# Kernel optimization log

Measured on AMD Instinct MI355X. Metric: run time of the kernel, lower is better.

Reference implementation:

```python
import jax, jax.numpy as jnp
import numpy as np

L1 = 3072
L2 = 15
L3 = 32
COUNT = 8
KAN_G = 3   # grid intervals
KAN_K = 3   # spline order


def _bspline_basis(x, grid, k):
    """Cox-de Boor B-spline basis. x: [B, in], grid: [in, G+2k+1] -> [B, in, G+k]."""
    x = x[:, :, None]                      # [B, in, 1]
    g = grid[None]                         # [1, in, M]
    B0 = ((x >= g[:, :, :-1]) & (x < g[:, :, 1:])).astype(x.dtype)
    for d in range(1, k + 1):
        B0 = ((x - g[:, :, : -(d + 1)]) / (g[:, :, d:-1] - g[:, :, : -(d + 1)]) * B0[:, :, :-1]
              + (g[:, :, d + 1:] - x) / (g[:, :, d + 1:] - g[:, :, 1:-d]) * B0[:, :, 1:])
    return B0  # [B, in, G+k]


def setup_inputs() -> dict:
    key = jax.random.key(0)
    ks = jax.random.split(key, 9)
    B = 16384
    in_dim = L2 * 2            # 30
    out_dim = L3 * COUNT       # 256
    x = jax.random.normal(ks[0], (B, L1), jnp.float32) * 0.1
    ls_indices = jax.random.randint(ks[1], (B,), 0, COUNT, dtype=jnp.int32)
    l1_w = jax.random.normal(ks[2], ((L2 + 1) * COUNT, L1), jnp.float32) / np.sqrt(L1).astype(np.float32)
    l1_b = jax.random.normal(ks[3], ((L2 + 1) * COUNT,), jnp.float32) * 0.01
    l1f_w = jax.random.normal(ks[4], (L2 + 1, L1), jnp.float32) / np.sqrt(L1).astype(np.float32)
    l1f_b = jnp.zeros((L2 + 1,), jnp.float32)
    # KAN layer: uniform extended grid on [-1,1], G+2k+1 = 10 knots per input dim
    h = 2.0 / KAN_G
    g1 = jnp.arange(-KAN_K, KAN_G + KAN_K + 1, dtype=jnp.float32) * h - 1.0
    kan_grid = jnp.tile(g1[None], (in_dim, 1))                      # [30, 10]
    kan_coef = jax.random.normal(ks[5], (in_dim, out_dim, KAN_G + KAN_K), jnp.float32) * 0.1
    kan_scale_base = jax.random.normal(ks[6], (in_dim, out_dim), jnp.float32) / np.sqrt(in_dim).astype(np.float32)
    kan_scale_sp = jnp.ones((in_dim, out_dim), jnp.float32)
    out_w = jax.random.normal(ks[7], (COUNT, L3), jnp.float32) / np.sqrt(L3).astype(np.float32)
    out_b = jnp.zeros((COUNT,), jnp.float32)
    return dict(x=x, ls_indices=ls_indices, l1_w=l1_w, l1_b=l1_b, l1f_w=l1f_w, l1f_b=l1f_b,
                kan_grid=kan_grid, kan_coef=kan_coef, kan_scale_base=kan_scale_base,
                kan_scale_sp=kan_scale_sp, out_w=out_w, out_b=out_b)


def reference(x, ls_indices, l1_w, l1_b, l1f_w, l1f_b, kan_grid, kan_coef,
              kan_scale_base, kan_scale_sp, out_w, out_b):
    B = x.shape[0]
    idx = ls_indices.reshape(-1) + jnp.arange(B, dtype=ls_indices.dtype) * COUNT  # [B]
    # l1: dense over all stacks, then gather the selected stack row per sample
    l1s = (x @ l1_w.T + l1_b).reshape(B * COUNT, L2 + 1)
    l1c = l1s[idx]                                  # [B, L2+1]
    l1f = x @ l1f_w.T + l1f_b                       # [B, L2+1]
    l1c_, l1c_out = l1c[:, :L2], l1c[:, L2:]
    l1f_, l1f_out = l1f[:, :L2], l1f[:, L2:]
    l1x = l1c_ + l1f_                               # [B, L2]
    l1x = jnp.clip(jnp.concatenate([l1x * l1x * (127.0 / 128.0), l1x], axis=1), 0.0, 1.0)  # [B, 2*L2]
    # KAN layer (single KANLayer, 30 -> 256): silu base + B-spline, summed over inputs
    basis = _bspline_basis(l1x, kan_grid, KAN_K)    # [B, 30, G+k]
    w_sp = kan_coef * kan_scale_sp[:, :, None]      # fold scale into coef -> [30, 256, G+k]
    l2s = (jnp.einsum('bi,io->bo', jax.nn.silu(l1x), kan_scale_base)
           + jnp.einsum('bik,iok->bo', basis, w_sp))  # [B, 256]
    l2c = l2s.reshape(B * COUNT, L3)[idx]           # [B, L3]
    l2x = jnp.clip(l2c, 0.0, 1.0)
    l3s = (l2x @ out_w.T + out_b).reshape(B * COUNT, 1)
    l3c = l3s[idx]                                  # [B, 1]
    return l3c + l1f_out + l1c_out
```

## Files before the change

kernel.cpp:

```cpp
#include <hip/hip_runtime.h>
#include <hip/hip_bf16.h>
#include <math.h>

#define NB 16384
#define KD 3072
#define TPB 256

typedef __attribute__((ext_vector_type(8))) short bf16x8;
typedef __attribute__((ext_vector_type(4))) float f32x4;

#define WS_W_OFF 66816
#define WS_WK_OFF 951552

__device__ __forceinline__ unsigned short f2bf(float f) {
    unsigned u = __float_as_uint(f);
    u += 0x7FFFu + ((u >> 16) & 1u);
    return (unsigned short)(u >> 16);
}

__global__ void k0a(const float* __restrict__ l1_w, const float* __restrict__ l1f_w,
                    unsigned short* __restrict__ W) {
    int g = blockIdx.x * TPB + threadIdx.x;
    int e = g * 4;
    const float* src = (e < 128 * KD) ? (l1_w + e) : (l1f_w + (e - 128 * KD));
    float4 v = *(const float4*)src;
    int2 o;
    o.x = (unsigned)f2bf(v.x) | ((unsigned)f2bf(v.y) << 16);
    o.y = (unsigned)f2bf(v.z) | ((unsigned)f2bf(v.w) << 16);
    *(int2*)(W + e) = o;
}

__global__ void k0b(const float* __restrict__ coef, const float* __restrict__ sb,
                    const float* __restrict__ sp, unsigned short* __restrict__ Wk,
                    int* __restrict__ meta) {
    int o = blockIdx.x;
    int k = threadIdx.x;
    if (o == 0 && k < 16) meta[k] = 0;
    if (k >= 224) return;
    float val = 0.f;
    if (k < 30) {
        val = sb[k * 256 + o];
    } else if (k >= 32 && k < 212) {
        int t = k - 32;
        int i = t / 6;
        int kk = t - i * 6;
        val = coef[((size_t)i * 256 + o) * 6 + kk] * sp[i * 256 + o];
    }
    Wk[o * 224 + k] = f2bf(val);
}

__global__ void k1a(const int* __restrict__ ls, int* __restrict__ meta) {
    int r = blockIdx.x * TPB + threadIdx.x;
    int bb = ls[r];
    int lane = threadIdx.x & 63;
    for (int q = 0; q < 8; q++) {
        unsigned long long mask = __ballot(bb == q);
        if (mask != 0ull) {
            int leader = __ffsll((unsigned long long)mask) - 1;
            if (lane == leader) atomicAdd(&meta[q], (int)__popcll(mask));
        }
    }
}

__global__ void k1b(int* __restrict__ meta) {
    if (threadIdx.x == 0 && blockIdx.x == 0) {
        int po = 0;
        for (int q = 0; q < 8; q++) {
            meta[16 + q] = po;
            po += (meta[q] + 31) & ~31;
        }
        meta[24] = po;
    }
}

__global__ void k1c(const int* __restrict__ ls, int* __restrict__ meta) {
    int r = blockIdx.x * TPB + threadIdx.x;
    int bb = ls[r];
    int lane = threadIdx.x & 63;
    int* cursor = meta + 8;
    const int* po = meta + 16;
    int* idxL = meta + 32;
    for (int q = 0; q < 8; q++) {
        unsigned long long mask = __ballot(bb == q);
        if (mask != 0ull) {
            int leader = __ffsll((unsigned long long)mask) - 1;
            int base = 0;
            if (lane == leader) base = atomicAdd(&cursor[q], (int)__popcll(mask));
            base = __shfl(base, leader);
            if (bb == q) {
                int rank = (int)__popcll(mask & ((1ull << lane) - 1ull));
                idxL[po[q] + base + rank] = r;
            }
        }
    }
}

__global__ __launch_bounds__(TPB, 2) void k2_main(
    const float* __restrict__ x, const int* __restrict__ meta,
    const unsigned short* __restrict__ W, const unsigned short* __restrict__ WkG,
    const float* __restrict__ l1_b, const float* __restrict__ l1f_b,
    const float* __restrict__ out_w, const float* __restrict__ out_b,
    float* __restrict__ out)
{
    __shared__ int s_po[9];
    __shared__ int s_rows[32];
    __shared__ int s_valid[32];
    __shared__ unsigned short Ab[32][64];
    __shared__ unsigned short Bb[32][64];
    __shared__ float hS[32][33];
    __shared__ unsigned short uL[32][232];
    __shared__ unsigned short WkS[32][232];
    __shared__ float sPart[2][32];

    int tid = threadIdx.x;
    if (tid < 9) s_po[tid] = meta[16 + tid];
    __syncthreads();
    int slot0 = blockIdx.x * 32;
    if (slot0 >= s_po[8]) return;
    int b = 0;
    while (b < 7 && slot0 >= s_po[b + 1]) b++;
    int bcnt = meta[b];
    if (tid < 32) {
        int slot = slot0 + tid;
        int rel = slot - s_po[b];
        int valid = (rel < bcnt) ? 1 : 0;
        const int* idxL = meta + 32;
        s_rows[tid] = idxL[valid ? slot : s_po[b]];
        s_valid[tid] = valid;
    }
    __syncthreads();

    int w = tid >> 6, lane = tid & 63;
    int mt = w & 1, nt = w >> 1;
    int quad = lane >> 4, l16 = lane & 15;
    int sm = tid >> 3, seg = tid & 7;

    const float4* xp = (const float4*)(x + (size_t)s_rows[sm] * KD) + seg * 2;
    int wrow = (sm < 16) ? (b * 16 + sm) : (112 + sm);
    const int4* wp = (const int4*)(W + (size_t)wrow * KD) + seg;

    unsigned short* aWr = &Ab[sm][(seg ^ (sm & 7)) * 8];
    unsigned short* bWr = &Bb[sm][(seg ^ (sm & 7)) * 8];
    int arow = mt * 16 + l16;
    int brow = nt * 16 + l16;

    f32x4 acc = {0.f, 0.f, 0.f, 0.f};
    for (int kt = 0; kt < 48; kt++) {
        float4 a0 = xp[kt * 16];
        float4 a1 = xp[kt * 16 + 1];
        int4 bv = wp[kt * 8];
        int4 av;
        av.x = (unsigned)f2bf(a0.x) | ((unsigned)f2bf(a0.y) << 16);
        av.y = (unsigned)f2bf(a0.z) | ((unsigned)f2bf(a0.w) << 16);
        av.z = (unsigned)f2bf(a1.x) | ((unsigned)f2bf(a1.y) << 16);
        av.w = (unsigned)f2bf(a1.z) | ((unsigned)f2bf(a1.w) << 16);
        __syncthreads();
        *(int4*)aWr = av;
        *(int4*)bWr = bv;
        __syncthreads();
#pragma unroll
        for (int ks = 0; ks < 2; ks++) {
            int blkA = ((ks * 4 + quad) ^ (arow & 7)) * 8;
            int blkB = ((ks * 4 + quad) ^ (brow & 7)) * 8;
            bf16x8 af = *(const bf16x8*)(&Ab[arow][blkA]);
            bf16x8 bfv = *(const bf16x8*)(&Bb[brow][blkB]);
            acc = __builtin_amdgcn_mfma_f32_16x16x32_bf16(af, bfv, acc, 0, 0, 0);
        }
    }

    {
        int col = nt * 16 + l16;
        float bias = (col < 16) ? l1_b[b * 16 + col] : l1f_b[col - 16];
        int rbase = mt * 16 + quad * 4;
        hS[rbase + 0][col] = acc[0] + bias;
        hS[rbase + 1][col] = acc[1] + bias;
        hS[rbase + 2][col] = acc[2] + bias;
        hS[rbase + 3][col] = acc[3] + bias;
    }
    __syncthreads();

    if (tid < 32) {
        unsigned* z = (unsigned*)&uL[tid][212];
        z[0] = 0; z[1] = 0; z[2] = 0; z[3] = 0; z[4] = 0; z[5] = 0;
        *(unsigned*)&uL[tid][30] = 0;
    }
    for (int item = tid; item < 480; item += TPB) {
        int row = item / 15;
        int ii = item - row * 15;
        float v = hS[row][ii] + hS[row][16 + ii];
        float xs = fminf(v * v * (127.f / 128.f), 1.f);
        float xl = fminf(fmaxf(v, 0.f), 1.f);
#pragma unroll
        for (int which = 0; which < 2; which++) {
            float xv = which ? xl : xs;
            int i = which ? (15 + ii) : ii;
            float sg = 1.f / (1.f + __expf(-xv));
            uL[row][i] = f2bf(xv * sg);
            float s = xv * 1.5f + 4.5f;
            int j = (int)s;
            float f = s - (float)j;
            float omf = 1.f - f;
            float f2 = f * f, f3 = f2 * f;
            float N0 = omf * omf * omf * (1.f / 6.f);
            float N1 = (3.f * f3 - 6.f * f2 + 4.f) * (1.f / 6.f);
            float N2 = (-3.f * f3 + 3.f * f2 + 3.f * f + 1.f) * (1.f / 6.f);
            float N3 = f3 * (1.f / 6.f);
            float b1 = (j == 4) ? N0 : 0.f;
            float b2 = (j == 4) ? N1 : ((j == 5) ? N0 : 0.f);
            float b3 = (j == 4) ? N2 : ((j == 5) ? N1 : N0);
            float b4 = (j == 4) ? N3 : ((j == 5) ? N2 : N1);
            float b5 = (j == 5) ? N3 : ((j == 6) ? N2 : 0.f);
            unsigned* dst = (unsigned*)&uL[row][32 + i * 6];
            dst[0] = ((unsigned)f2bf(b1) << 16);
            dst[1] = (unsigned)f2bf(b2) | ((unsigned)f2bf(b3) << 16);
            dst[2] = (unsigned)f2bf(b4) | ((unsigned)f2bf(b5) << 16);
        }
    }
    for (int c = tid; c < 448; c += TPB) {
        int row = c / 14;
        int cc = c - row * 14;
        const int4* src = (const int4*)(WkG + ((size_t)(b * 32 + row)) * 224 + cc * 16);
        int4 v0 = src[0];
        int4 v1 = src[1];
        int4* dst = (int4*)&WkS[row][cc * 16];
        dst[0] = v0;
        dst[1] = v1;
    }
    __syncthreads();

    f32x4 acc2 = {0.f, 0.f, 0.f, 0.f};
    const unsigned short* uRd = &uL[mt * 16 + l16][quad * 8];
    const unsigned short* wRd = &WkS[nt * 16 + l16][quad * 8];
#pragma unroll
    for (int ks = 0; ks < 7; ks++) {
        bf16x8 uf = *(const bf16x8*)(uRd + ks * 32);
        bf16x8 wf = *(const bf16x8*)(wRd + ks * 32);
        acc2 = __builtin_amdgcn_mfma_f32_16x16x32_bf16(uf, wf, acc2, 0, 0, 0);
    }

    float ow = out_w[b * 32 + nt * 16 + l16];
    float p0 = fminf(fmaxf(acc2[0], 0.f), 1.f) * ow;
    float p1 = fminf(fmaxf(acc2[1], 0.f), 1.f) * ow;
    float p2 = fminf(fmaxf(acc2[2], 0.f), 1.f) * ow;
    float p3 = fminf(fmaxf(acc2[3], 0.f), 1.f) * ow;
#pragma unroll
    for (int off = 1; off < 16; off <<= 1) {
        p0 += __shfl_xor(p0, off);
        p1 += __shfl_xor(p1, off);
        p2 += __shfl_xor(p2, off);
        p3 += __shfl_xor(p3, off);
    }
    if (l16 == 0) {
        int rbase = mt * 16 + quad * 4;
        sPart[nt][rbase + 0] = p0;
        sPart[nt][rbase + 1] = p1;
        sPart[nt][rbase + 2] = p2;
        sPart[nt][rbase + 3] = p3;
    }
    __syncthreads();
    if (tid < 32 && s_valid[tid]) {
        float res = sPart[0][tid] + sPart[1][tid] + out_b[b] + hS[tid][15] + hS[tid][31];
        out[s_rows[tid]] = res;
    }
}

extern "C" void kernel_launch(void* const* d_in, const int* in_sizes, int n_in,
                              void* d_out, int out_size, void* d_ws, size_t ws_size,
                              hipStream_t stream) {
    (void)in_sizes; (void)n_in; (void)out_size; (void)ws_size;
    const float* x     = (const float*)d_in[0];
    const int*   ls    = (const int*)d_in[1];
    const float* l1_w  = (const float*)d_in[2];
    const float* l1_b  = (const float*)d_in[3];
    const float* l1f_w = (const float*)d_in[4];
    const float* l1f_b = (const float*)d_in[5];
    const float* coef  = (const float*)d_in[7];
    const float* sb    = (const float*)d_in[8];
    const float* sp    = (const float*)d_in[9];
    const float* ow    = (const float*)d_in[10];
    const float* ob    = (const float*)d_in[11];
    float* out = (float*)d_out;

    char* ws = (char*)d_ws;
    int* meta = (int*)ws;
    unsigned short* W  = (unsigned short*)(ws + WS_W_OFF);
    unsigned short* Wk = (unsigned short*)(ws + WS_WK_OFF);

    hipLaunchKernelGGL(k0a, dim3(432), dim3(TPB), 0, stream, l1_w, l1f_w, W);
    hipLaunchKernelGGL(k0b, dim3(256), dim3(TPB), 0, stream, coef, sb, sp, Wk, meta);
    hipLaunchKernelGGL(k1a, dim3(64), dim3(TPB), 0, stream, ls, meta);
    hipLaunchKernelGGL(k1b, dim3(1), dim3(64), 0, stream, meta);
    hipLaunchKernelGGL(k1c, dim3(64), dim3(TPB), 0, stream, ls, meta);
    hipLaunchKernelGGL(k2_main, dim3(520), dim3(TPB), 0, stream,
                       x, meta, W, Wk, l1_b, l1f_b, ow, ob, out);
}
```

Baseline: 366.2 us.

## Fuse preprocessing kernels and double-buffer the main GEMM loop with register prefetch

Merges the weight-conversion, KAN-weight packing and histogram kernels into one launch, with per-block partial counts replacing global atomics and reduced in k1b. The main GEMM loop now double-buffers its LDS tiles and prefetches the next k-tiles into registers, dropping one barrier per step. LDS is aliased between the GEMM buffers and the KAN stage, and launch bounds are raised to 3 blocks per SM to lift occupancy. This trades more register pressure for better latency hiding.

```diff
diff --git a/kernel.cpp b/kernel.cpp
--- a/kernel.cpp
+++ b/kernel.cpp
@@ -9,8 +9,9 @@
 typedef __attribute__((ext_vector_type(8))) short bf16x8;
 typedef __attribute__((ext_vector_type(4))) float f32x4;
 
-#define WS_W_OFF 66816
-#define WS_WK_OFF 951552
+#define WS_PART_OFF 66688
+#define WS_W_OFF 69632
+#define WS_WK_OFF 954368
 
 __device__ __forceinline__ unsigned short f2bf(float f) {
     unsigned u = __float_as_uint(f);
@@ -18,56 +19,73 @@
     return (unsigned short)(u >> 16);
 }
 
-__global__ void k0a(const float* __restrict__ l1_w, const float* __restrict__ l1f_w,
-                    unsigned short* __restrict__ W) {
-    int g = blockIdx.x * TPB + threadIdx.x;
-    int e = g * 4;
-    const float* src = (e < 128 * KD) ? (l1_w + e) : (l1f_w + (e - 128 * KD));
-    float4 v = *(const float4*)src;
-    int2 o;
-    o.x = (unsigned)f2bf(v.x) | ((unsigned)f2bf(v.y) << 16);
-    o.y = (unsigned)f2bf(v.z) | ((unsigned)f2bf(v.w) << 16);
-    *(int2*)(W + e) = o;
-}
-
-__global__ void k0b(const float* __restrict__ coef, const float* __restrict__ sb,
-                    const float* __restrict__ sp, unsigned short* __restrict__ Wk,
-                    int* __restrict__ meta) {
-    int o = blockIdx.x;
-    int k = threadIdx.x;
-    if (o == 0 && k < 16) meta[k] = 0;
-    if (k >= 224) return;
-    float val = 0.f;
-    if (k < 30) {
-        val = sb[k * 256 + o];
-    } else if (k >= 32 && k < 212) {
-        int t = k - 32;
-        int i = t / 6;
-        int kk = t - i * 6;
-        val = coef[((size_t)i * 256 + o) * 6 + kk] * sp[i * 256 + o];
-    }
-    Wk[o * 224 + k] = f2bf(val);
-}
-
-__global__ void k1a(const int* __restrict__ ls, int* __restrict__ meta) {
-    int r = blockIdx.x * TPB + threadIdx.x;
-    int bb = ls[r];
-    int lane = threadIdx.x & 63;
-    for (int q = 0; q < 8; q++) {
-        unsigned long long mask = __ballot(bb == q);
-        if (mask != 0ull) {
-            int leader = __ffsll((unsigned long long)mask) - 1;
-            if (lane == leader) atomicAdd(&meta[q], (int)__popcll(mask));
-        }
-    }
-}
-
-__global__ void k1b(int* __restrict__ meta) {
-    if (threadIdx.x == 0 && blockIdx.x == 0) {
+__global__ void k_pre(const float* __restrict__ l1_w, const float* __restrict__ l1f_w,
+                      unsigned short* __restrict__ W,
+                      const float* __restrict__ coef, const float* __restrict__ sb,
+                      const float* __restrict__ sp, unsigned short* __restrict__ Wk,
+                      const int* __restrict__ ls, int* __restrict__ part) {
+    __shared__ int cnt[8];
+    int bid = blockIdx.x;
+    int tid = threadIdx.x;
+    if (bid < 432) {
+        int g = bid * TPB + tid;
+        int e = g * 4;
+        const float* src = (e < 128 * KD) ? (l1_w + e) : (l1f_w + (e - 128 * KD));
+        float4 v = *(const float4*)src;
+        int2 o;
+        o.x = (unsigned)f2bf(v.x) | ((unsigned)f2bf(v.y) << 16);
+        o.y = (unsigned)f2bf(v.z) | ((unsigned)f2bf(v.w) << 16);
+        *(int2*)(W + e) = o;
+    } else if (bid < 688) {
+        int o = bid - 432;
+        int k = tid;
+        if (k < 224) {
+            float val = 0.f;
+            if (k < 30) {
+                val = sb[k * 256 + o];
+            } else if (k >= 32 && k < 212) {
+                int t = k - 32;
+                int i = t / 6;
+                int kk = t - i * 6;
+                val = coef[((size_t)i * 256 + o) * 6 + kk] * sp[i * 256 + o];
+            }
+            Wk[o * 224 + k] = f2bf(val);
+        }
+    } else {
+        int j = bid - 688;
+        int r = j * TPB + tid;
+        int bb = ls[r];
+        if (tid < 8) cnt[tid] = 0;
+        __syncthreads();
+        int lane = tid & 63;
+        for (int q = 0; q < 8; q++) {
+            unsigned long long mask = __ballot(bb == q);
+            if (mask != 0ull) {
+                int leader = __ffsll((unsigned long long)mask) - 1;
+                if (lane == leader) atomicAdd(&cnt[q], (int)__popcll(mask));
+            }
+        }
+        __syncthreads();
+        if (tid < 8) part[j * 8 + tid] = cnt[tid];
+    }
+}
+
+__global__ void k1b(const int* __restrict__ part, int* __restrict__ meta) {
+    __shared__ int sc[8];
+    int tid = threadIdx.x;
+    if (tid < 8) {
+        int s = 0;
+        for (int j = 0; j < 64; j++) s += part[j * 8 + tid];
+        sc[tid] = s;
+        meta[tid] = s;
+        meta[8 + tid] = 0;
+    }
+    __syncthreads();
+    if (tid == 0) {
         int po = 0;
         for (int q = 0; q < 8; q++) {
             meta[16 + q] = po;
-            po += (meta[q] + 31) & ~31;
+            po += (sc[q] + 31) & ~31;
         }
         meta[24] = po;
     }
@@ -95,7 +113,7 @@
     }
 }
 
-__global__ __launch_bounds__(TPB, 2) void k2_main(
+__global__ __launch_bounds__(TPB, 3) void k2_main(
     const float* __restrict__ x, const int* __restrict__ meta,
     const unsigned short* __restrict__ W, const unsigned short* __restrict__ WkG,
     const float* __restrict__ l1_b, const float* __restrict__ l1f_b,
@@ -105,12 +123,14 @@
     __shared__ int s_po[9];
     __shared__ int s_rows[32];
     __shared__ int s_valid[32];
-    __shared__ unsigned short Ab[32][64];
-    __shared__ unsigned short Bb[32][64];
     __shared__ float hS[32][33];
-    __shared__ unsigned short uL[32][232];
-    __shared__ unsigned short WkS[32][232];
     __shared__ float sPart[2][32];
+    __shared__ char smem[29696];
+
+    unsigned short* Abuf = (unsigned short*)smem;
+    unsigned short* Bbuf = (unsigned short*)(smem + 8192);
+    unsigned short* uL   = (unsigned short*)smem;
+    unsigned short* WkS  = (unsigned short*)(smem + 14848);
 
     int tid = threadIdx.x;
     if (tid < 9) s_po[tid] = meta[16 + tid];
@@ -139,32 +159,64 @@
     int wrow = (sm < 16) ? (b * 16 + sm) : (112 + sm);
     const int4* wp = (const int4*)(W + (size_t)wrow * KD) + seg;
 
-    unsigned short* aWr = &Ab[sm][(seg ^ (sm & 7)) * 8];
-    unsigned short* bWr = &Bb[sm][(seg ^ (sm & 7)) * 8];
+    int wrOff = sm * 64 + ((seg ^ (sm & 7)) * 8);
     int arow = mt * 16 + l16;
     int brow = nt * 16 + l16;
+    int rdA = arow * 64;
+    int rdB = brow * 64;
+
+    float4 a00 = xp[0],  a01 = xp[1];  int4 b0 = wp[0];
+    float4 a10 = xp[16], a11 = xp[17]; int4 b1 = wp[8];
 
     f32x4 acc = {0.f, 0.f, 0.f, 0.f};
-    for (int kt = 0; kt < 48; kt++) {
-        float4 a0 = xp[kt * 16];
-        float4 a1 = xp[kt * 16 + 1];
-        int4 bv = wp[kt * 8];
-        int4 av;
-        av.x = (unsigned)f2bf(a0.x) | ((unsigned)f2bf(a0.y) << 16);
-        av.y = (unsigned)f2bf(a0.z) | ((unsigned)f2bf(a0.w) << 16);
-        av.z = (unsigned)f2bf(a1.x) | ((unsigned)f2bf(a1.y) << 16);
-        av.w = (unsigned)f2bf(a1.z) | ((unsigned)f2bf(a1.w) << 16);
-        __syncthreads();
-        *(int4*)aWr = av;
-        *(int4*)bWr = bv;
-        __syncthreads();
-#pragma unroll
-        for (int ks = 0; ks < 2; ks++) {
-            int blkA = ((ks * 4 + quad) ^ (arow & 7)) * 8;
-            int blkB = ((ks * 4 + quad) ^ (brow & 7)) * 8;
-            bf16x8 af = *(const bf16x8*)(&Ab[arow][blkA]);
-            bf16x8 bfv = *(const bf16x8*)(&Bb[brow][blkB]);
-            acc = __builtin_amdgcn_mfma_f32_16x16x32_bf16(af, bfv, acc, 0, 0, 0);
+    for (int kt = 0; kt < 48; kt += 2) {
+        {
+            int4 av;
+            av.x = (unsigned)f2bf(a00.x) | ((unsigned)f2bf(a00.y) << 16);
+            av.y = (unsigned)f2bf(a00.z) | ((unsigned)f2bf(a00.w) << 16);
+            av.z = (unsigned)f2bf(a01.x) | ((unsigned)f2bf(a01.y) << 16);
+            av.w = (unsigned)f2bf(a01.z) | ((unsigned)f2bf(a01.w) << 16);
+            int4 bv = b0;
+            if (kt < 46) {
+                a00 = xp[(kt + 2) * 16];
+                a01 = xp[(kt + 2) * 16 + 1];
+                b0  = wp[(kt + 2) * 8];
+            }
+            *(int4*)(Abuf + wrOff) = av;
+            *(int4*)(Bbuf + wrOff) = bv;
+            __syncthreads();
+#pragma unroll
+            for (int ks = 0; ks < 2; ks++) {
+                int blkA = ((ks * 4 + quad) ^ (arow & 7)) * 8;
+                int blkB = ((ks * 4 + quad) ^ (brow & 7)) * 8;
+                bf16x8 af  = *(const bf16x8*)(Abuf + rdA + blkA);
+                bf16x8 bfv = *(const bf16x8*)(Bbuf + rdB + blkB);
+                acc = __builtin_amdgcn_mfma_f32_16x16x32_bf16(af, bfv, acc, 0, 0, 0);
+            }
+        }
+        {
+            int4 av;
+            av.x = (unsigned)f2bf(a10.x) | ((unsigned)f2bf(a10.y) << 16);
+            av.y = (unsigned)f2bf(a10.z) | ((unsigned)f2bf(a10.w) << 16);
+            av.z = (unsigned)f2bf(a11.x) | ((unsigned)f2bf(a11.y) << 16);
+            av.w = (unsigned)f2bf(a11.z) | ((unsigned)f2bf(a11.w) << 16);
+            int4 bv = b1;
+            if (kt < 45) {
+                a10 = xp[(kt + 3) * 16];
+                a11 = xp[(kt + 3) * 16 + 1];
+                b1  = wp[(kt + 3) * 8];
+            }
+            *(int4*)(Abuf + 2048 + wrOff) = av;
+            *(int4*)(Bbuf + 2048 + wrOff) = bv;
+            __syncthreads();
+#pragma unroll
+            for (int ks = 0; ks < 2; ks++) {
+                int blkA = ((ks * 4 + quad) ^ (arow & 7)) * 8;
+                int blkB = ((ks * 4 + quad) ^ (brow & 7)) * 8;
+                bf16x8 af  = *(const bf16x8*)(Abuf + 2048 + rdA + blkA);
+                bf16x8 bfv = *(const bf16x8*)(Bbuf + 2048 + rdB + blkB);
+                acc = __builtin_amdgcn_mfma_f32_16x16x32_bf16(af, bfv, acc, 0, 0, 0);
+            }
         }
     }
 
@@ -180,9 +232,9 @@
     __syncthreads();
 
     if (tid < 32) {
-        unsigned* z = (unsigned*)&uL[tid][212];
+        unsigned* z = (unsigned*)(uL + tid * 232 + 212);
         z[0] = 0; z[1] = 0; z[2] = 0; z[3] = 0; z[4] = 0; z[5] = 0;
-        *(unsigned*)&uL[tid][30] = 0;
+        *(unsigned*)(uL + tid * 232 + 30) = 0;
     }
     for (int item = tid; item < 480; item += TPB) {
         int row = item / 15;
@@ -195,7 +247,7 @@
             float xv = which ? xl : xs;
             int i = which ? (15 + ii) : ii;
             float sg = 1.f / (1.f + __expf(-xv));
-            uL[row][i] = f2bf(xv * sg);
+            uL[row * 232 + i] = f2bf(xv * sg);
             float s = xv * 1.5f + 4.5f;
             int j = (int)s;
             float f = s - (float)j;
@@ -210,7 +262,7 @@
             float b3 = (j == 4) ? N2 : ((j == 5) ? N1 : N0);
             float b4 = (j == 4) ? N3 : ((j == 5) ? N2 : N1);
             float b5 = (j == 5) ? N3 : ((j == 6) ? N2 : 0.f);
-            unsigned* dst = (unsigned*)&uL[row][32 + i * 6];
+            unsigned* dst = (unsigned*)(uL + row * 232 + 32 + i * 6);
             dst[0] = ((unsigned)f2bf(b1) << 16);
             dst[1] = (unsigned)f2bf(b2) | ((unsigned)f2bf(b3) << 16);
             dst[2] = (unsigned)f2bf(b4) | ((unsigned)f2bf(b5) << 16);
@@ -222,15 +274,15 @@
         const int4* src = (const int4*)(WkG + ((size_t)(b * 32 + row)) * 224 + cc * 16);
         int4 v0 = src[0];
         int4 v1 = src[1];
-        int4* dst = (int4*)&WkS[row][cc * 16];
+        int4* dst = (int4*)(WkS + row * 232 + cc * 16);
         dst[0] = v0;
         dst[1] = v1;
     }
     __syncthreads();
 
     f32x4 acc2 = {0.f, 0.f, 0.f, 0.f};
-    const unsigned short* uRd = &uL[mt * 16 + l16][quad * 8];
-    const unsigned short* wRd = &WkS[nt * 16 + l16][quad * 8];
+    const unsigned short* uRd = uL + (mt * 16 + l16) * 232 + quad * 8;
+    const unsigned short* wRd = WkS + (nt * 16 + l16) * 232 + quad * 8;
 #pragma unroll
     for (int ks = 0; ks < 7; ks++) {
         bf16x8 uf = *(const bf16x8*)(uRd + ks * 32);
@@ -283,13 +335,13 @@
 
     char* ws = (char*)d_ws;
     int* meta = (int*)ws;
+    int* part = (int*)(ws + WS_PART_OFF);
     unsigned short* W  = (unsigned short*)(ws + WS_W_OFF);
     unsigned short* Wk = (unsigned short*)(ws + WS_WK_OFF);
 
-    hipLaunchKernelGGL(k0a, dim3(432), dim3(TPB), 0, stream, l1_w, l1f_w, W);
-    hipLaunchKernelGGL(k0b, dim3(256), dim3(TPB), 0, stream, coef, sb, sp, Wk, meta);
-    hipLaunchKernelGGL(k1a, dim3(64), dim3(TPB), 0, stream, ls, meta);
-    hipLaunchKernelGGL(k1b, dim3(1), dim3(64), 0, stream, meta);
+    hipLaunchKernelGGL(k_pre, dim3(752), dim3(TPB), 0, stream,
+                       l1_w, l1f_w, W, coef, sb, sp, Wk, ls, part);
+    hipLaunchKernelGGL(k1b, dim3(1), dim3(64), 0, stream, part, meta);
     hipLaunchKernelGGL(k1c, dim3(64), dim3(TPB), 0, stream, ls, meta);
     hipLaunchKernelGGL(k2_main, dim3(520), dim3(TPB), 0, stream,
                        x, meta, W, Wk, l1_b, l1f_b, ow, ob, out);
```

Result: faster. 349.0 us (-4.7%).
